# Performance work log

Measured on AMD Instinct MI355X. Metric: run time of the kernel, lower is better.

## Reference

```python
import jax, jax.numpy as jnp
import numpy as np

B, N, DIM, H = 2, 2048, 1024, 16
D = DIM // H  # head_dim = 64


def setup_inputs() -> dict:
    key = jax.random.key(0)
    ks = jax.random.split(key, 3)
    w_scale = 0.02
    return {
        "x": jax.random.normal(ks[0], (B, N, DIM), dtype=jnp.float32),
        "Wqkv": jax.random.normal(ks[1], (DIM, 3 * DIM), dtype=jnp.float32) * w_scale,
        "bqkv": jnp.zeros((3 * DIM,), dtype=jnp.float32),
        "Wproj": jax.random.normal(ks[2], (DIM, DIM), dtype=jnp.float32) * w_scale,
        "bproj": jnp.zeros((DIM,), dtype=jnp.float32),
        "sigma": jnp.ones((1,), dtype=jnp.float32),
        "gamma": jnp.ones((1,), dtype=jnp.float32),
    }


def reference(x, Wqkv, bqkv, Wproj, bproj, sigma, gamma):
    b, n, c = x.shape
    # qkv projection -> (B, N, 3, H, D)
    qkv = (x @ Wqkv + bqkv).reshape(b, n, 3, H, D)
    q = jnp.transpose(qkv[:, :, 0], (0, 2, 1, 3))  # [B, H, N, D]
    k = jnp.transpose(qkv[:, :, 1], (0, 2, 1, 3))
    v = jnp.transpose(qkv[:, :, 2], (0, 2, 1, 3))
    scale = 1.0 / jnp.sqrt(jnp.asarray(D, dtype=x.dtype))
    scores = jnp.einsum("bhqd,bhkd->bhqk", q, k) * scale  # [B, H, N, N]
    # divisive normalization (cortical gain control) over key axis
    denom = sigma + jnp.sqrt(jnp.mean(scores * scores, axis=-1, keepdims=True))
    scores = gamma * scores / denom
    attn = jax.nn.softmax(scores, axis=-1)
    out = jnp.einsum("bhqk,bhkd->bhqd", attn, v)  # [B, H, N, D]
    out = jnp.transpose(out, (0, 2, 1, 3)).reshape(b, n, c)
    return out @ Wproj + bproj
```

## Files before the change

kernel.cpp:

```cpp
#include <hip/hip_runtime.h>

typedef __attribute__((ext_vector_type(4))) float f32x4;
typedef __attribute__((ext_vector_type(8))) _Float16 f16x8;
typedef __attribute__((ext_vector_type(4))) _Float16 f16x4;
typedef __attribute__((ext_vector_type(2))) _Float16 f16x2;

#define MFMA_F16(a, b, c) __builtin_amdgcn_mfma_f32_16x16x32_f16(a, b, c, 0, 0, 0)

__device__ __forceinline__ void gload_lds16(const void* g, void* l) {
  __builtin_amdgcn_global_load_lds(
      (const __attribute__((address_space(1))) void*)g,
      (__attribute__((address_space(3))) void*)l, 16, 0, 0);
}
__device__ __forceinline__ f16x2 pk2(float a, float b) {
  return __builtin_bit_cast(f16x2, __builtin_amdgcn_cvt_pkrtz(a, b));
}
__device__ __forceinline__ void pipe_barrier_v4() {
  asm volatile("s_waitcnt vmcnt(4) lgkmcnt(0)" ::: "memory");
  __builtin_amdgcn_sched_barrier(0);
  __builtin_amdgcn_s_barrier();
}
__device__ __forceinline__ void pipe_barrier_v2() {
  asm volatile("s_waitcnt vmcnt(2) lgkmcnt(0)" ::: "memory");
  __builtin_amdgcn_sched_barrier(0);
  __builtin_amdgcn_s_barrier();
}
__device__ __forceinline__ void pipe_barrier_v0() {
  asm volatile("s_waitcnt vmcnt(0) lgkmcnt(0)" ::: "memory");
  __builtin_amdgcn_sched_barrier(0);
  __builtin_amdgcn_s_barrier();
}

__global__ __launch_bounds__(256) void prep_kernel(
    const float* __restrict__ x, _Float16* __restrict__ xf,
    const float* __restrict__ Wqkv, _Float16* __restrict__ wqt,
    const float* __restrict__ Wproj, _Float16* __restrict__ wpt) {
  __shared__ float tile[32][33];
  const int bx = blockIdx.x;
  if (bx < 4096) {
    const int i = bx * 256 + threadIdx.x;
    f32x4 v = *(const f32x4*)(x + (size_t)i * 4);
    f16x4 h;
#pragma unroll
    for (int j = 0; j < 4; ++j) h[j] = (_Float16)v[j];
    *(f16x4*)(xf + (size_t)i * 4) = h;
    return;
  }
  const float* W;
  _Float16* wt;
  int N, n0, k0;
  if (bx < 7168) {
    const int t = bx - 4096;
    W = Wqkv; wt = wqt; N = 3072;
    n0 = (t % 96) * 32; k0 = (t / 96) * 32;
  } else {
    const int t = bx - 7168;
    W = Wproj; wt = wpt; N = 1024;
    n0 = (t % 32) * 32; k0 = (t / 32) * 32;
  }
  const int tx = threadIdx.x & 31, ty = threadIdx.x >> 5;
#pragma unroll
  for (int j = 0; j < 32; j += 8)
    tile[ty + j][tx] = W[(size_t)(k0 + ty + j) * N + n0 + tx];
  __syncthreads();
#pragma unroll
  for (int j = 0; j < 32; j += 8)
    wt[(size_t)(n0 + ty + j) * 1024 + k0 + tx] = (_Float16)tile[tx][ty + j];
}

__global__ __launch_bounds__(256) void gemm_qkv_kernel(
    const _Float16* __restrict__ xf, const _Float16* __restrict__ wt,
    const float* __restrict__ bias, _Float16* __restrict__ QF,
    _Float16* __restrict__ KF, _Float16* __restrict__ KT,
    _Float16* __restrict__ VT) {
  __shared__ __attribute__((aligned(16))) _Float16 lg[24576];
  const int tid = threadIdx.x, lane = tid & 63, w = tid >> 6;
  const int wg = blockIdx.x;
  const int cx = wg & 7, c = wg >> 3;
  const int bxl = (cx & 1) * 12 + c % 12;
  const int byl = (cx >> 1) * 8 + c / 12;
  const int m0 = byl * 128, n0 = bxl * 128;
  const int wr = (w >> 1) * 64, wc = (w & 1) * 64;
  f32x4 acc[4][4] = {};

  const int srow = lane >> 2;
  const int scol = (((lane & 3) ^ ((lane >> 3) & 3)) * 8);
  const int fr = lane & 15, fg = lane >> 4;
  const int rswz = (fr >> 1) & 3;

  auto stageT = [&](int buf, int k0) {
#pragma unroll
    for (int j = 0; j < 2; ++j) {
      const int rbase = 32 * w + 16 * j;
      const int r = rbase + srow;
      gload_lds16(xf + (size_t)(m0 + r) * 1024 + k0 + scol,
                  &lg[buf * 8192 + rbase * 32]);
      gload_lds16(wt + (size_t)(n0 + r) * 1024 + k0 + scol,
                  &lg[buf * 8192 + 4096 + rbase * 32]);
    }
  };

  stageT(0, 0);
  stageT(1, 32);
  pipe_barrier_v4();
  int cur = 0;
  for (int t = 0; t < 32; ++t) {
    if (t < 30) {
      const int nb = (cur + 2 >= 3) ? cur - 1 : cur + 2;
      stageT(nb, (t + 2) * 32);
    }
    const int ab = cur * 8192;
    f16x8 af[4], bfr[4];
#pragma unroll
    for (int m = 0; m < 4; ++m)
      af[m] = *(const f16x8*)&lg[ab + (wr + 16 * m + fr) * 32 + ((fg ^ rswz) * 8)];
#pragma unroll
    for (int n = 0; n < 4; ++n)
      bfr[n] = *(const f16x8*)&lg[ab + 4096 + (wc + 16 * n + fr) * 32 + ((fg ^ rswz) * 8)];
#pragma unroll
    for (int m = 0; m < 4; ++m)
#pragma unroll
      for (int n = 0; n < 4; ++n) acc[m][n] = MFMA_F16(af[m], bfr[n], acc[m][n]);
    if (t < 30) pipe_barrier_v4(); else pipe_barrier_v0();
    cur = (cur + 1 == 3) ? 0 : cur + 1;
  }

  const int fq = fg * 4;
#pragma unroll
  for (int n = 0; n < 4; ++n) {
    const float bv = bias[n0 + wc + 16 * n + fr];
#pragma unroll
    for (int m = 0; m < 4; ++m)
#pragma unroll
      for (int i = 0; i < 4; ++i)
        lg[(wr + 16 * m + fq + i) * 129 + wc + 16 * n + fr] =
            (_Float16)(acc[m][n][i] + bv);
  }
  __syncthreads();
  const int b = m0 >> 11, nnb = m0 & 2047;
  const int h0 = 2 * (bxl & 7);
  const int sPhase = bxl >> 3;
  if (sPhase <= 1) {
    _Float16* __restrict__ dst = (sPhase == 0) ? QF : KF;
#pragma unroll
    for (int p = 0; p < 8; ++p) {
      const int r = p * 16 + (tid >> 4);
      const int cc = tid & 15;
      f16x8 vals;
#pragma unroll
      for (int j = 0; j < 8; ++j) vals[j] = lg[r * 129 + cc * 8 + j];
      const int h = cc >> 3, d = (cc & 7) * 8;
      *(f16x8*)&dst[((size_t)((b * 16 + h0 + h) * 2048 + nnb + r)) * 64 + d] = vals;
    }
  }
  if (sPhase >= 1) {
    _Float16* __restrict__ T = (sPhase == 1) ? KT : VT;
#pragma unroll
    for (int p = 0; p < 8; ++p) {
      const int lr = p * 16 + (tid >> 4);
      const int cc = tid & 15;
      f16x8 vals;
#pragma unroll
      for (int j = 0; j < 8; ++j) vals[j] = lg[(cc * 8 + j) * 129 + lr];
      const int h = lr >> 6, d = lr & 63;
      *(f16x8*)&T[((size_t)((b * 16 + h0 + h) * 64 + d)) * 2048 + nnb + cc * 8] = vals;
    }
  }
}

__global__ __launch_bounds__(256) void gram_kernel(
    const _Float16* __restrict__ KT, _Float16* __restrict__ GH,
    _Float16* __restrict__ GL) {
  __shared__ __attribute__((aligned(16))) _Float16 sT[3][4096];
  const int tid = threadIdx.x, lane = tid & 63, w = tid >> 6;
  const int bh = blockIdx.x;
  const _Float16* src = KT + (size_t)bh * 64 * 2048;
  const int s_r = lane >> 3, s_cg = lane & 7;
  const int fr = lane & 15, fg = lane >> 4;
  const int kswz = fr & 7;

  auto stage = [&](int buf, int n0) {
#pragma unroll
    for (int j = 0; j < 2; ++j) {
      const int rbase = 8 * w + 32 * j;
      gload_lds16(src + (size_t)(rbase + s_r) * 2048 + n0 + ((s_cg ^ s_r) * 8),
                  &sT[buf][rbase * 64]);
    }
  };

  f32x4 acc[4] = {};
  stage(0, 0);
  stage(1, 64);
  pipe_barrier_v2();
  int cur = 0;
  for (int t = 0; t < 32; ++t) {
    if (t < 30) {
      const int nb = (cur + 2 >= 3) ? cur - 1 : cur + 2;
      stage(nb, (t + 2) * 64);
    }
    f16x8 af[2];
#pragma unroll
    for (int ks = 0; ks < 2; ++ks)
      af[ks] = *(const f16x8*)&sT[cur][(16 * w + fr) * 64 + (((ks * 4 + fg) ^ kswz) * 8)];
#pragma unroll
    for (int nt = 0; nt < 4; ++nt)
#pragma unroll
      for (int ks = 0; ks < 2; ++ks)
        acc[nt] = MFMA_F16(
            af[ks],
            *(const f16x8*)&sT[cur][(16 * nt + fr) * 64 + (((ks * 4 + fg) ^ kswz) * 8)],
            acc[nt]);
    if (t < 30) pipe_barrier_v2(); else pipe_barrier_v0();
    cur = (cur + 1 == 3) ? 0 : cur + 1;
  }
#pragma unroll
  for (int nt = 0; nt < 4; ++nt) {
#pragma unroll
    for (int i = 0; i < 4; ++i) {
      const float g = acc[nt][i];
      const _Float16 gh = (_Float16)g;
      const size_t o = (size_t)bh * 4096 + (16 * w + fg * 4 + i) * 64 + 16 * nt + fr;
      GH[o] = gh;
      GL[o] = (_Float16)(g - (float)gh);
    }
  }
}

__global__ __launch_bounds__(256) void attn_kernel(
    const _Float16* __restrict__ QF, const _Float16* __restrict__ KF,
    const _Float16* __restrict__ VT, const _Float16* __restrict__ GH,
    const _Float16* __restrict__ GL, _Float16* __restrict__ OB,
    const float* __restrict__ sigma_p, const float* __restrict__ gamma_p) {
  __shared__ __attribute__((aligned(16))) _Float16 lds[24576];

  const int tid = threadIdx.x, lane = tid & 63, w = tid >> 6;
  const int wg = blockIdx.x;
  const int c = wg >> 3;
  const int bh = (wg & 7) * 4 + (c >> 4);
  const int q0 = (c & 15) * 128;
  const size_t base = (size_t)bh * (2048 * 64);
  const float sigma = sigma_p[0], gamma = gamma_p[0];
  const int fr = lane & 15, fg = lane >> 4;
  const int s_r = lane >> 3, s_cg = lane & 7;
  const int kswz = fr & 7;

  const _Float16* Kbh = KF + base;
  const _Float16* Tbh = VT + base;

  f16x8 qf[2][2];
#pragma unroll
  for (int m = 0; m < 2; ++m)
#pragma unroll
    for (int ks = 0; ks < 2; ++ks)
      qf[m][ks] = *(const f16x8*)(QF + base +
                                  (size_t)(q0 + 32 * w + 16 * m + fr) * 64 +
                                  ks * 32 + fg * 8);

  auto stage64 = [&](int dstoff, const _Float16* g, int srcstride) {
#pragma unroll
    for (int j = 0; j < 2; ++j) {
      const int rbase = 8 * w + 32 * j;
      gload_lds16(g + (size_t)(rbase + s_r) * srcstride + ((s_cg ^ s_r) * 8),
                  &lds[dstoff + rbase * 64]);
    }
  };
  auto stage64K = [&](int dstoff, const _Float16* g) {
#pragma unroll
    for (int j = 0; j < 2; ++j) {
      const int rbase = 8 * w + 32 * j;
      const int r = rbase + s_r;
      const int pr = (r & 0x23) | ((r & 0x0C) << 1) | ((r & 0x10) >> 2);
      gload_lds16(g + (size_t)pr * 64 + ((s_cg ^ s_r) * 8),
                  &lds[dstoff + rbase * 64]);
    }
  };

  stage64(0, GH + (size_t)bh * 4096, 64);
  stage64(4096, GL + (size_t)bh * 4096, 64);
  __syncthreads();
  float minvl2[2];
  float* Yp = (float*)&lds[8192 + w * 2048];
#pragma unroll
  for (int m = 0; m < 2; ++m) {
    f32x4 yacc[4] = {};
#pragma unroll
    for (int nt = 0; nt < 4; ++nt) {
#pragma unroll
      for (int ks = 0; ks < 2; ++ks) {
        const int off = (16 * nt + fr) * 64 + (((ks * 4 + fg) ^ kswz) * 8);
        yacc[nt] = MFMA_F16(qf[m][ks], *(const f16x8*)&lds[off], yacc[nt]);
        yacc[nt] = MFMA_F16(qf[m][ks], *(const f16x8*)&lds[4096 + off], yacc[nt]);
      }
    }
#pragma unroll
    for (int nt = 0; nt < 4; ++nt)
#pragma unroll
      for (int i = 0; i < 4; ++i) Yp[(fg * 4 + i) * 64 + 16 * nt + fr] = yacc[nt][i];
    float zp = 0.0f;
#pragma unroll
    for (int ks = 0; ks < 2; ++ks) {
      const f32x4 y0 = *(const f32x4*)&Yp[fr * 64 + ks * 32 + fg * 8];
      const f32x4 y1 = *(const f32x4*)&Yp[fr * 64 + ks * 32 + fg * 8 + 4];
#pragma unroll
      for (int cc = 0; cc < 4; ++cc) {
        zp += y0[cc] * (float)qf[m][ks][cc];
        zp += y1[cc] * (float)qf[m][ks][cc + 4];
      }
    }
    zp += __shfl_xor(zp, 16);
    zp += __shfl_xor(zp, 32);
    const float rms = sqrtf(fmaxf(zp, 0.0f)) * (1.0f / 362.038672f);
    minvl2[m] = gamma / (sigma + rms) * 0.125f * 1.44269504f;
  }
  __syncthreads();

  float lsum[2] = {};
  f32x4 oacc[2][4] = {};
  stage64K(0, Kbh);
  stage64(12288, Tbh, 2048);
  stage64K(4096, Kbh + 64 * 64);
  stage64(16384, Tbh + 64, 2048);
  pipe_barrier_v4();
  int cur = 0;
  for (int kb = 0; kb < 32; ++kb) {
    if (kb < 30) {
      const int nb = (cur + 2 >= 3) ? cur - 1 : cur + 2;
      stage64K(nb * 4096, Kbh + (size_t)(kb + 2) * 64 * 64);
      stage64(12288 + nb * 4096, Tbh + (kb + 2) * 64, 2048);
    }
    const int koff = cur * 4096, voff = 12288 + cur * 4096;
    f32x4 pacc[2][4];
#pragma unroll
    for (int n = 0; n < 4; ++n) {
      const int offb = koff + (16 * n + fr) * 64;
      const f16x8 kf0 = *(const f16x8*)&lds[offb + ((fg ^ kswz) * 8)];
      const f16x8 kf1 = *(const f16x8*)&lds[offb + (((4 + fg) ^ kswz) * 8)];
#pragma unroll
      for (int m = 0; m < 2; ++m) {
        f32x4 a = {};
        a = MFMA_F16(kf0, qf[m][0], a);
        a = MFMA_F16(kf1, qf[m][1], a);
        pacc[m][n] = a;
      }
    }
#pragma unroll
    for (int m = 0; m < 2; ++m)
#pragma unroll
      for (int n = 0; n < 4; ++n)
#pragma unroll
        for (int i = 0; i < 4; ++i) {
          const float p = __builtin_amdgcn_exp2f(pacc[m][n][i] * minvl2[m]);
          lsum[m] += p;
          pacc[m][n][i] = p;
        }
#pragma unroll
    for (int ks2 = 0; ks2 < 2; ++ks2) {
      f16x8 bf[2];
#pragma unroll
      for (int m = 0; m < 2; ++m) {
        const f16x2 c0 = pk2(pacc[m][2 * ks2][0], pacc[m][2 * ks2][1]);
        const f16x2 c1 = pk2(pacc[m][2 * ks2][2], pacc[m][2 * ks2][3]);
        const f16x2 c2 = pk2(pacc[m][2 * ks2 + 1][0], pacc[m][2 * ks2 + 1][1]);
        const f16x2 c3 = pk2(pacc[m][2 * ks2 + 1][2], pacc[m][2 * ks2 + 1][3]);
        bf[m][0] = c0[0]; bf[m][1] = c0[1]; bf[m][2] = c1[0]; bf[m][3] = c1[1];
        bf[m][4] = c2[0]; bf[m][5] = c2[1]; bf[m][6] = c3[0]; bf[m][7] = c3[1];
      }
#pragma unroll
      for (int nf = 0; nf < 4; ++nf) {
        const int off = voff + (16 * nf + fr) * 64 + (((ks2 * 4 + fg) ^ kswz) * 8);
        const f16x8 vt = *(const f16x8*)&lds[off];
        oacc[0][nf] = MFMA_F16(vt, bf[0], oacc[0][nf]);
        oacc[1][nf] = MFMA_F16(vt, bf[1], oacc[1][nf]);
      }
    }
    if (kb < 30) pipe_barrier_v4(); else pipe_barrier_v0();
    cur = (cur + 1 == 3) ? 0 : cur + 1;
  }
  float inv[2];
#pragma unroll
  for (int m = 0; m < 2; ++m) {
    lsum[m] += __shfl_xor(lsum[m], 16);
    lsum[m] += __shfl_xor(lsum[m], 32);
    inv[m] = 1.0f / lsum[m];
  }

  const int b = bh >> 4, h = bh & 15;
#pragma unroll
  for (int m = 0; m < 2; ++m) {
    const size_t orow = (size_t)(b * 2048 + q0 + 32 * w + 16 * m + fr);
#pragma unroll
    for (int nf = 0; nf < 4; ++nf) {
      f16x4 ov;
#pragma unroll
      for (int i = 0; i < 4; ++i) ov[i] = (_Float16)(oacc[m][nf][i] * inv[m]);
      *(f16x4*)&OB[orow * 1024 + h * 64 + 16 * nf + 4 * fg] = ov;
    }
  }
}

__global__ __launch_bounds__(256) void gemm_proj_kernel(
    const _Float16* __restrict__ A, const _Float16* __restrict__ Bt,
    const float* __restrict__ bias, float* __restrict__ out) {
  __shared__ __attribute__((aligned(16))) _Float16 lg[24576];
  const int tid = threadIdx.x, lane = tid & 63, w = tid >> 6;
  const int wg = blockIdx.x;
  const int c = wg >> 3;
  const int bxl = c & 7;
  const int byl = (wg & 7) * 4 + (c >> 3);
  const int m0 = byl * 128, n0 = bxl * 128;
  const int wr = (w >> 1) * 64, wc = (w & 1) * 64;
  f32x4 acc[4][4] = {};
  const int srow = lane >> 2;
  const int scol = (((lane & 3) ^ ((lane >> 3) & 3)) * 8);
  const int fr = lane & 15, fg = lane >> 4;
  const int rswz = (fr >> 1) & 3;

  auto stageT = [&](int buf, int k0) {
#pragma unroll
    for (int j = 0; j < 2; ++j) {
      const int rbase = 32 * w + 16 * j;
      const int r = rbase + srow;
      gload_lds16(A + (size_t)(m0 + r) * 1024 + k0 + scol,
                  &lg[buf * 8192 + rbase * 32]);
      gload_lds16(Bt + (size_t)(n0 + r) * 1024 + k0 + scol,
                  &lg[buf * 8192 + 4096 + rbase * 32]);
    }
  };

  stageT(0, 0);
  stageT(1, 32);
  pipe_barrier_v4();
  int cur = 0;
  for (int t = 0; t < 32; ++t) {
    if (t < 30) {
      const int nb = (cur + 2 >= 3) ? cur - 1 : cur + 2;
      stageT(nb, (t + 2) * 32);
    }
    const int ab = cur * 8192;
    f16x8 af[4], bfr[4];
#pragma unroll
    for (int m = 0; m < 4; ++m)
      af[m] = *(const f16x8*)&lg[ab + (wr + 16 * m + fr) * 32 + ((fg ^ rswz) * 8)];
#pragma unroll
    for (int n = 0; n < 4; ++n)
      bfr[n] = *(const f16x8*)&lg[ab + 4096 + (wc + 16 * n + fr) * 32 + ((fg ^ rswz) * 8)];
#pragma unroll
    for (int m = 0; m < 4; ++m)
#pragma unroll
      for (int n = 0; n < 4; ++n) acc[m][n] = MFMA_F16(af[m], bfr[n], acc[m][n]);
    if (t < 30) pipe_barrier_v4(); else pipe_barrier_v0();
    cur = (cur + 1 == 3) ? 0 : cur + 1;
  }
  const int fq = fg * 4;
#pragma unroll
  for (int n = 0; n < 4; ++n) {
    const int col = n0 + wc + 16 * n + fr;
    const float bv = bias[col];
#pragma unroll
    for (int m = 0; m < 4; ++m) {
#pragma unroll
      for (int i = 0; i < 4; ++i) {
        const int row = m0 + wr + 16 * m + fq + i;
        out[(size_t)row * 1024 + col] = acc[m][n][i] + bv;
      }
    }
  }
}

extern "C" void kernel_launch(void* const* d_in, const int* in_sizes, int n_in,
                              void* d_out, int out_size, void* d_ws, size_t ws_size,
                              hipStream_t stream) {
  const float* x = (const float*)d_in[0];
  const float* Wqkv = (const float*)d_in[1];
  const float* bqkv = (const float*)d_in[2];
  const float* Wproj = (const float*)d_in[3];
  const float* bproj = (const float*)d_in[4];
  const float* sigma = (const float*)d_in[5];
  const float* gamma = (const float*)d_in[6];
  float* out = (float*)d_out;

  char* ws = (char*)d_ws;
  const size_t MB = 1024 * 1024;
  _Float16* XF  = (_Float16*)(ws + 0 * MB);
  _Float16* WQT = (_Float16*)(ws + 8 * MB);
  _Float16* WPT = (_Float16*)(ws + 14 * MB);
  _Float16* QF  = (_Float16*)(ws + 16 * MB);
  _Float16* KF  = (_Float16*)(ws + 24 * MB);
  _Float16* VT  = (_Float16*)(ws + 32 * MB);
  _Float16* KT  = (_Float16*)(ws + 40 * MB);
  _Float16* OB  = (_Float16*)(ws + 40 * MB);
  _Float16* GH  = (_Float16*)(ws + 8 * MB);
  _Float16* GL  = (_Float16*)(ws + 8 * MB + 512 * 1024);

  prep_kernel<<<8192, 256, 0, stream>>>(x, XF, Wqkv, WQT, Wproj, WPT);
  gemm_qkv_kernel<<<768, 256, 0, stream>>>(XF, WQT, bqkv, QF, KF, KT, VT);
  gram_kernel<<<32, 256, 0, stream>>>(KT, GH, GL);
  attn_kernel<<<512, 256, 0, stream>>>(QF, KF, VT, GH, GL, OB, sigma, gamma);
  gemm_proj_kernel<<<256, 256, 0, stream>>>(OB, WPT, bproj, out);
}
```

Baseline: 126.2 us.

## Double-buffer attention K/V in pairs with setprio, halve proj GEMM M-tile

The attention kernel's three-slot ring of K/V tiles becomes a double buffer holding pairs of 64-key tiles. Each step loads two tiles at once and has one full barrier per pair instead of one per tile. s_setprio is raised around the MFMA sections. The projection GEMM tile shrinks from 128x128 to 64x128 and the grid doubles to 512 blocks, so more CUs stay busy, at the cost of more B-matrix reloads and the larger attention LDS footprint.

```diff
diff --git a/kernel.cpp b/kernel.cpp
--- a/kernel.cpp
+++ b/kernel.cpp
@@ -17,6 +17,11 @@
 }
 __device__ __forceinline__ void pipe_barrier_v4() {
   asm volatile("s_waitcnt vmcnt(4) lgkmcnt(0)" ::: "memory");
+  __builtin_amdgcn_sched_barrier(0);
+  __builtin_amdgcn_s_barrier();
+}
+__device__ __forceinline__ void pipe_barrier_v3() {
+  asm volatile("s_waitcnt vmcnt(3) lgkmcnt(0)" ::: "memory");
   __builtin_amdgcn_sched_barrier(0);
   __builtin_amdgcn_s_barrier();
 }
@@ -231,7 +236,7 @@
     const _Float16* __restrict__ VT, const _Float16* __restrict__ GH,
     const _Float16* __restrict__ GL, _Float16* __restrict__ OB,
     const float* __restrict__ sigma_p, const float* __restrict__ gamma_p) {
-  __shared__ __attribute__((aligned(16))) _Float16 lds[24576];
+  __shared__ __attribute__((aligned(16))) _Float16 lds[32768];
 
   const int tid = threadIdx.x, lane = tid & 63, w = tid >> 6;
   const int wg = blockIdx.x;
@@ -317,64 +322,73 @@
   float lsum[2] = {};
   f32x4 oacc[2][4] = {};
   stage64K(0, Kbh);
-  stage64(12288, Tbh, 2048);
-  stage64K(4096, Kbh + 64 * 64);
-  stage64(16384, Tbh + 64, 2048);
-  pipe_barrier_v4();
-  int cur = 0;
-  for (int kb = 0; kb < 32; ++kb) {
-    if (kb < 30) {
-      const int nb = (cur + 2 >= 3) ? cur - 1 : cur + 2;
-      stage64K(nb * 4096, Kbh + (size_t)(kb + 2) * 64 * 64);
-      stage64(12288 + nb * 4096, Tbh + (kb + 2) * 64, 2048);
-    }
-    const int koff = cur * 4096, voff = 12288 + cur * 4096;
-    f32x4 pacc[2][4];
-#pragma unroll
-    for (int n = 0; n < 4; ++n) {
-      const int offb = koff + (16 * n + fr) * 64;
-      const f16x8 kf0 = *(const f16x8*)&lds[offb + ((fg ^ kswz) * 8)];
-      const f16x8 kf1 = *(const f16x8*)&lds[offb + (((4 + fg) ^ kswz) * 8)];
-#pragma unroll
-      for (int m = 0; m < 2; ++m) {
-        f32x4 a = {};
-        a = MFMA_F16(kf0, qf[m][0], a);
-        a = MFMA_F16(kf1, qf[m][1], a);
-        pacc[m][n] = a;
+  stage64(16384, Tbh, 2048);
+  stage64K(4096, Kbh + 4096);
+  stage64(20480, Tbh + 64, 2048);
+  pipe_barrier_v0();
+  for (int g = 0; g < 16; ++g) {
+    if (g < 15) {
+      const int qb = ((g + 1) & 1) * 2;
+      const int t2 = 2 * g + 2;
+      stage64K(qb * 4096, Kbh + (size_t)t2 * 4096);
+      stage64(16384 + qb * 4096, Tbh + t2 * 64, 2048);
+      stage64K((qb + 1) * 4096, Kbh + (size_t)(t2 + 1) * 4096);
+      stage64(16384 + (qb + 1) * 4096, Tbh + (t2 + 1) * 64, 2048);
+    }
+    const int pb = (g & 1) * 2;
+#pragma unroll
+    for (int tt = 0; tt < 2; ++tt) {
+      const int koff = (pb + tt) * 4096, voff = 16384 + (pb + tt) * 4096;
+      f32x4 pacc[2][4];
+      __builtin_amdgcn_s_setprio(1);
+#pragma unroll
+      for (int n = 0; n < 4; ++n) {
+        const int offb = koff + (16 * n + fr) * 64;
+        const f16x8 kf0 = *(const f16x8*)&lds[offb + ((fg ^ kswz) * 8)];
+        const f16x8 kf1 = *(const f16x8*)&lds[offb + (((4 + fg) ^ kswz) * 8)];
+#pragma unroll
+        for (int m = 0; m < 2; ++m) {
+          f32x4 a = {};
+          a = MFMA_F16(kf0, qf[m][0], a);
+          a = MFMA_F16(kf1, qf[m][1], a);
+          pacc[m][n] = a;
+        }
       }
-    }
-#pragma unroll
-    for (int m = 0; m < 2; ++m)
-#pragma unroll
-      for (int n = 0; n < 4; ++n)
-#pragma unroll
-        for (int i = 0; i < 4; ++i) {
-          const float p = __builtin_amdgcn_exp2f(pacc[m][n][i] * minvl2[m]);
-          lsum[m] += p;
-          pacc[m][n][i] = p;
+      __builtin_amdgcn_s_setprio(0);
+#pragma unroll
+      for (int m = 0; m < 2; ++m)
+#pragma unroll
+        for (int n = 0; n < 4; ++n)
+#pragma unroll
+          for (int i = 0; i < 4; ++i) {
+            const float p = __builtin_amdgcn_exp2f(pacc[m][n][i] * minvl2[m]);
+            lsum[m] += p;
+            pacc[m][n][i] = p;
+          }
+#pragma unroll
+      for (int ks2 = 0; ks2 < 2; ++ks2) {
+        f16x8 bf[2];
+#pragma unroll
+        for (int m = 0; m < 2; ++m) {
+          const f16x2 c0 = pk2(pacc[m][2 * ks2][0], pacc[m][2 * ks2][1]);
+          const f16x2 c1 = pk2(pacc[m][2 * ks2][2], pacc[m][2 * ks2][3]);
+          const f16x2 c2 = pk2(pacc[m][2 * ks2 + 1][0], pacc[m][2 * ks2 + 1][1]);
+          const f16x2 c3 = pk2(pacc[m][2 * ks2 + 1][2], pacc[m][2 * ks2 + 1][3]);
+          bf[m][0] = c0[0]; bf[m][1] = c0[1]; bf[m][2] = c1[0]; bf[m][3] = c1[1];
+          bf[m][4] = c2[0]; bf[m][5] = c2[1]; bf[m][6] = c3[0]; bf[m][7] = c3[1];
         }
-#pragma unroll
-    for (int ks2 = 0; ks2 < 2; ++ks2) {
-      f16x8 bf[2];
-#pragma unroll
-      for (int m = 0; m < 2; ++m) {
-        const f16x2 c0 = pk2(pacc[m][2 * ks2][0], pacc[m][2 * ks2][1]);
-        const f16x2 c1 = pk2(pacc[m][2 * ks2][2], pacc[m][2 * ks2][3]);
-        const f16x2 c2 = pk2(pacc[m][2 * ks2 + 1][0], pacc[m][2 * ks2 + 1][1]);
-        const f16x2 c3 = pk2(pacc[m][2 * ks2 + 1][2], pacc[m][2 * ks2 + 1][3]);
-        bf[m][0] = c0[0]; bf[m][1] = c0[1]; bf[m][2] = c1[0]; bf[m][3] = c1[1];
-        bf[m][4] = c2[0]; bf[m][5] = c2[1]; bf[m][6] = c3[0]; bf[m][7] = c3[1];
+        __builtin_amdgcn_s_setprio(1);
+#pragma unroll
+        for (int nf = 0; nf < 4; ++nf) {
+          const int off = voff + (16 * nf + fr) * 64 + (((ks2 * 4 + fg) ^ kswz) * 8);
+          const f16x8 vt = *(const f16x8*)&lds[off];
+          oacc[0][nf] = MFMA_F16(vt, bf[0], oacc[0][nf]);
+          oacc[1][nf] = MFMA_F16(vt, bf[1], oacc[1][nf]);
+        }
+        __builtin_amdgcn_s_setprio(0);
       }
-#pragma unroll
-      for (int nf = 0; nf < 4; ++nf) {
-        const int off = voff + (16 * nf + fr) * 64 + (((ks2 * 4 + fg) ^ kswz) * 8);
-        const f16x8 vt = *(const f16x8*)&lds[off];
-        oacc[0][nf] = MFMA_F16(vt, bf[0], oacc[0][nf]);
-        oacc[1][nf] = MFMA_F16(vt, bf[1], oacc[1][nf]);
-      }
-    }
-    if (kb < 30) pipe_barrier_v4(); else pipe_barrier_v0();
-    cur = (cur + 1 == 3) ? 0 : cur + 1;
+    }
+    pipe_barrier_v0();
   }
   float inv[2];
 #pragma unroll
@@ -401,54 +415,56 @@
 __global__ __launch_bounds__(256) void gemm_proj_kernel(
     const _Float16* __restrict__ A, const _Float16* __restrict__ Bt,
     const float* __restrict__ bias, float* __restrict__ out) {
-  __shared__ __attribute__((aligned(16))) _Float16 lg[24576];
+  __shared__ __attribute__((aligned(16))) _Float16 lg[18432];
   const int tid = threadIdx.x, lane = tid & 63, w = tid >> 6;
   const int wg = blockIdx.x;
   const int c = wg >> 3;
   const int bxl = c & 7;
-  const int byl = (wg & 7) * 4 + (c >> 3);
-  const int m0 = byl * 128, n0 = bxl * 128;
-  const int wr = (w >> 1) * 64, wc = (w & 1) * 64;
-  f32x4 acc[4][4] = {};
+  const int byl = (wg & 7) * 8 + (c >> 3);
+  const int m0 = byl * 64, n0 = bxl * 128;
+  const int wr = (w >> 1) * 32, wc = (w & 1) * 64;
+  f32x4 acc[2][4] = {};
   const int srow = lane >> 2;
   const int scol = (((lane & 3) ^ ((lane >> 3) & 3)) * 8);
   const int fr = lane & 15, fg = lane >> 4;
   const int rswz = (fr >> 1) & 3;
 
   auto stageT = [&](int buf, int k0) {
+    {
+      const int rbase = 16 * w;
+      gload_lds16(A + (size_t)(m0 + rbase + srow) * 1024 + k0 + scol,
+                  &lg[buf * 6144 + rbase * 32]);
+    }
 #pragma unroll
     for (int j = 0; j < 2; ++j) {
       const int rbase = 32 * w + 16 * j;
-      const int r = rbase + srow;
-      gload_lds16(A + (size_t)(m0 + r) * 1024 + k0 + scol,
-                  &lg[buf * 8192 + rbase * 32]);
-      gload_lds16(Bt + (size_t)(n0 + r) * 1024 + k0 + scol,
-                  &lg[buf * 8192 + 4096 + rbase * 32]);
+      gload_lds16(Bt + (size_t)(n0 + rbase + srow) * 1024 + k0 + scol,
+                  &lg[buf * 6144 + 2048 + rbase * 32]);
     }
   };
 
   stageT(0, 0);
   stageT(1, 32);
-  pipe_barrier_v4();
+  pipe_barrier_v3();
   int cur = 0;
   for (int t = 0; t < 32; ++t) {
     if (t < 30) {
       const int nb = (cur + 2 >= 3) ? cur - 1 : cur + 2;
       stageT(nb, (t + 2) * 32);
     }
-    const int ab = cur * 8192;
-    f16x8 af[4], bfr[4];
-#pragma unroll
-    for (int m = 0; m < 4; ++m)
+    const int ab = cur * 6144;
+    f16x8 af[2], bfr[4];
+#pragma unroll
+    for (int m = 0; m < 2; ++m)
       af[m] = *(const f16x8*)&lg[ab + (wr + 16 * m + fr) * 32 + ((fg ^ rswz) * 8)];
 #pragma unroll
     for (int n = 0; n < 4; ++n)
-      bfr[n] = *(const f16x8*)&lg[ab + 4096 + (wc + 16 * n + fr) * 32 + ((fg ^ rswz) * 8)];
-#pragma unroll
-    for (int m = 0; m < 4; ++m)
+      bfr[n] = *(const f16x8*)&lg[ab + 2048 + (wc + 16 * n + fr) * 32 + ((fg ^ rswz) * 8)];
+#pragma unroll
+    for (int m = 0; m < 2; ++m)
 #pragma unroll
       for (int n = 0; n < 4; ++n) acc[m][n] = MFMA_F16(af[m], bfr[n], acc[m][n]);
-    if (t < 30) pipe_barrier_v4(); else pipe_barrier_v0();
+    if (t < 30) pipe_barrier_v3(); else pipe_barrier_v0();
     cur = (cur + 1 == 3) ? 0 : cur + 1;
   }
   const int fq = fg * 4;
@@ -457,7 +473,7 @@
     const int col = n0 + wc + 16 * n + fr;
     const float bv = bias[col];
 #pragma unroll
-    for (int m = 0; m < 4; ++m) {
+    for (int m = 0; m < 2; ++m) {
 #pragma unroll
       for (int i = 0; i < 4; ++i) {
         const int row = m0 + wr + 16 * m + fq + i;
@@ -496,5 +512,5 @@
   gemm_qkv_kernel<<<768, 256, 0, stream>>>(XF, WQT, bqkv, QF, KF, KT, VT);
   gram_kernel<<<32, 256, 0, stream>>>(KT, GH, GL);
   attn_kernel<<<512, 256, 0, stream>>>(QF, KF, VT, GH, GL, OB, sigma, gamma);
-  gemm_proj_kernel<<<256, 256, 0, stream>>>(OB, WPT, bproj, out);
-}
+  gemm_proj_kernel<<<512, 256, 0, stream>>>(OB, WPT, bproj, out);
+}
```

New measurement: 128.0 us. Within noise of the previous version (+1.4%).
